# Optimization experiments

Hardware: AMD Instinct MI355X
Metric: run time of the kernel (lower is better)

## Reference

```python
import jax, jax.numpy as jnp
from jax import lax
import numpy as np

COMMITMENT_COST = 0.25
N_EMBED = 512
EDIM = 32


def _conv(x, w, b, stride, pad):
    # x: NCHW, w: OIHW (torch Conv2d layout)
    y = lax.conv_general_dilated(x, w, (stride, stride), [(pad, pad), (pad, pad)],
                                 dimension_numbers=("NCHW", "OIHW", "NCHW"))
    return y + b[None, :, None, None]


def _conv_t(x, w, b, stride, pad):
    # torch ConvTranspose2d weight layout: (in, out, kH, kW)
    k = w.shape[2]
    w_ = jnp.flip(w, (2, 3)).transpose(1, 0, 2, 3)  # -> OIHW
    p = k - 1 - pad
    y = lax.conv_general_dilated(x, w_, (1, 1), [(p, p), (p, p)],
                                 lhs_dilation=(stride, stride),
                                 dimension_numbers=("NCHW", "OIHW", "NCHW"))
    return y + b[None, :, None, None]


def setup_inputs() -> dict:
    key = jax.random.key(0)
    ks = jax.random.split(key, 9)
    rn = lambda k, s: jax.random.normal(k, s, jnp.float32) * 0.05
    return {
        "x": jax.random.normal(ks[0], (32, 3, 256, 256), jnp.float32),
        "e_w1": rn(ks[1], (64, 3, 4, 4)),    "e_b1": jnp.zeros((64,), jnp.float32),
        "e_w2": rn(ks[2], (128, 64, 4, 4)),  "e_b2": jnp.zeros((128,), jnp.float32),
        "e_w3": rn(ks[3], (32, 128, 3, 3)),  "e_b3": jnp.zeros((32,), jnp.float32),
        "embed": jax.random.uniform(ks[4], (N_EMBED, EDIM), jnp.float32,
                                    -1.0 / N_EMBED, 1.0 / N_EMBED),
        "d_w1": rn(ks[5], (32, 128, 3, 3)),  "d_b1": jnp.zeros((128,), jnp.float32),
        "d_w2": rn(ks[6], (128, 64, 4, 4)),  "d_b2": jnp.zeros((64,), jnp.float32),
        "d_w3": rn(ks[7], (64, 3, 4, 4)),    "d_b3": jnp.zeros((3,), jnp.float32),
    }


def reference(x, e_w1, e_b1, e_w2, e_b2, e_w3, e_b3, embed,
              d_w1, d_b1, d_w2, d_b2, d_w3, d_b3):
    # ---- encoder ----
    h = jax.nn.relu(_conv(x, e_w1, e_b1, 2, 1))   # [B,64,128,128]
    h = jax.nn.relu(_conv(h, e_w2, e_b2, 2, 1))   # [B,128,64,64]
    z = jax.nn.relu(_conv(h, e_w3, e_b3, 1, 1))   # [B,32,64,64]
    # ---- vector quantizer ----
    zp = z.transpose(0, 2, 3, 1)                  # BHWC
    zf = zp.reshape(-1, EDIM)                     # [N, 32]
    d = (zf ** 2).sum(1, keepdims=True) + (embed ** 2).sum(1) \
        - 2.0 * zf @ embed.T                      # [N, n_embed]
    idx = jnp.argmin(d, axis=1)                   # [N]
    z_q = embed[idx].reshape(zp.shape)            # gather == onehot @ embed
    sg = lax.stop_gradient
    loss = jnp.mean((sg(z_q) - zp) ** 2) + COMMITMENT_COST * jnp.mean((z_q - sg(zp)) ** 2)
    z_q_st = zp + sg(z_q - zp)                    # straight-through
    z_q_st = z_q_st.transpose(0, 3, 1, 2)         # back to NCHW
    # ---- decoder ----
    h = jax.nn.relu(_conv_t(z_q_st, d_w1, d_b1, 1, 1))  # [B,128,64,64]
    h = jax.nn.relu(_conv_t(h, d_w2, d_b2, 2, 1))       # [B,64,128,128]
    x_recon = _conv_t(h, d_w3, d_b3, 2, 1)              # [B,3,256,256]
    return x_recon, loss
```

## Files before the change

kernel.cpp:

```cpp
#include <hip/hip_runtime.h>


typedef __attribute__((ext_vector_type(8))) short     short8;
typedef __attribute__((ext_vector_type(4))) short     s16x4;
typedef __attribute__((ext_vector_type(8))) __bf16    bf16x8;
typedef __attribute__((ext_vector_type(4))) float     f32x4;
typedef __attribute__((ext_vector_type(4))) unsigned  uint32x4;

#define BATCH 32

__device__ __forceinline__ float b2f(unsigned short b) {
  union { unsigned u; float f; } v; v.u = ((unsigned)b) << 16; return v.f;
}
__device__ __forceinline__ unsigned short f2b(float f) {
  union { float f; unsigned u; } v; v.f = f;
  unsigned r = v.u + 0x7FFF + ((v.u >> 16) & 1);
  return (unsigned short)(r >> 16);
}

__global__ __launch_bounds__(256) void prep1v_k(const float* __restrict__ w,
                                                unsigned short* __restrict__ wq) {
  const int i = blockIdx.x*256 + threadIdx.x;
  const int j = i & 7, l = (i >> 3) & 63, ni = (i >> 9) & 3, ks = i >> 11;
  const int k = ks*32 + (l >> 4)*8 + j;
  const int co = ni*16 + (l & 15);
  wq[i] = (k < 48) ? f2b(w[co*48 + k]) : (unsigned short)0;
}
__global__ __launch_bounds__(256) void prep2v_k(const float* __restrict__ w,
                                                unsigned short* __restrict__ wq) {
  const int i = blockIdx.x*256 + threadIdx.x;
  const int j = i & 7, l = (i >> 3) & 63, ni = (i >> 9) & 7, ks = i >> 12;
  const int lm = l & 15, lk = l >> 4;
  const int tap = ks >> 1, cc = ks & 1;
  const int co = ni*16 + lm, ci = cc*32 + lk*8 + j;
  wq[i] = f2b(w[(co*64 + ci)*16 + tap]);
}
__global__ __launch_bounds__(256) void prep3_k(const float* __restrict__ w,
                                               unsigned short* __restrict__ wq) {
  const int i = blockIdx.x*256 + threadIdx.x;
  const int ci = i & 127, co = (i >> 7) & 31, t = i >> 12;
  wq[i] = f2b(w[(co*128 + ci)*9 + t]);
}
__global__ __launch_bounds__(256) void prep4_k(const float* __restrict__ w,
                                               unsigned short* __restrict__ wq) {
  const int i = blockIdx.x*256 + threadIdx.x;
  const int ci = i & 31, co = (i >> 5) & 127, t = i >> 12;
  wq[i] = f2b(w[(ci*128 + co)*9 + (8 - t)]);
}
__global__ __launch_bounds__(256) void prep5v_k(const float* __restrict__ w,
                                                unsigned short* __restrict__ wq) {
  const int i = blockIdx.x*256 + threadIdx.x;
  const int j = i & 7, l = (i >> 3) & 63, ni = (i >> 9) & 3;
  const int ks = (i >> 11) & 15, p = i >> 15;
  const int lm = l & 15, lk = l >> 4;
  const int py = p >> 1, px = p & 1;
  const int a = ks >> 3, b = (ks >> 2) & 1, cc = ks & 3;
  const int co = ni*16 + lm, ci = cc*32 + lk*8 + j;
  const int ky = 3 - 2*a - py, kx = 3 - 2*b - px;
  wq[i] = f2b(w[(ci*64 + co)*16 + ky*4 + kx]);
}
__global__ __launch_bounds__(256) void prep6_k(const float* __restrict__ w,
                                               unsigned short* __restrict__ wq) {
  const int i = blockIdx.x*256 + threadIdx.x;
  const int j = i & 7, l = (i >> 3) & 63, kc = (i >> 9) & 7, p = i >> 12;
  const int lm = l & 15, lk = l >> 4;
  const int a = kc >> 2, b = (kc >> 1) & 1, ch = kc & 1;
  const int ci = ch*32 + lk*8 + j, co = lm;
  const int py = p >> 1, px = p & 1;
  const int ky = 2 - 2*a + (1 - py), kx = 2 - 2*b + (1 - px);
  wq[i] = (co < 3) ? f2b(w[(ci*3 + co)*16 + ky*4 + kx]) : (unsigned short)0;
}

template<int CIN,int COUT,int HIN,int S,int KW,int NTAPS,int OSTRIDE,int P,
         bool PARITY,bool RELU,bool INF32,bool OUTF32>
__global__ __launch_bounds__(256) void mconv_k(const void* __restrict__ in_,
    const unsigned short* __restrict__ wq_, const float* __restrict__ bias,
    void* __restrict__ out_) {
  constexpr int NF  = COUT / 16;
  constexpr int NCH = CIN / 32;
  __shared__ short Al[128*40];
  __shared__ short Bl[COUT*40];
  int py = 0, px = 0, PY = P, PX = P;
  const unsigned short* wq = wq_;
  if (PARITY) {
    py = blockIdx.y >> 1; px = blockIdx.y & 1;
    PY = 1 - py; PX = 1 - px;
    wq += blockIdx.y * (NTAPS*COUT*CIN);
  }
  const int m0 = blockIdx.x * 128;
  const int w  = threadIdx.x >> 6, l = threadIdx.x & 63;
  const int lm = l & 15, lk = l >> 4;
  f32x4 acc[2][NF];
  #pragma unroll
  for (int mi = 0; mi < 2; ++mi)
    #pragma unroll
    for (int ni = 0; ni < NF; ++ni) acc[mi][ni] = (f32x4)0.0f;

  for (int tap = 0; tap < NTAPS; ++tap) {
    const int ky = tap / KW, kx = tap % KW;
    for (int ch = 0; ch < NCH; ++ch) {
      const int c0 = ch * 32;
      __syncthreads();
      for (int s = threadIdx.x; s < 512; s += 256) {
        const int row = s >> 2, part = s & 3;
        const int m = m0 + row;
        const int n = m >> 12, oy = (m >> 6) & 63, ox = m & 63;
        const int iy = oy*S - PY + ky, ix = ox*S - PX + kx;
        short8 v = (short8)(short)0;
        if (iy >= 0 && iy < HIN && ix >= 0 && ix < HIN) {
          const int base = ((n*HIN + iy)*HIN + ix)*CIN + c0 + part*8;
          if (INF32) {
            const float* pf = (const float*)in_ + base;
            const f32x4 f0 = *(const f32x4*)pf;
            const f32x4 f1 = *(const f32x4*)(pf + 4);
            #pragma unroll
            for (int j = 0; j < 4; ++j) {
              v[j]     = (short)f2b(f0[j]);
              v[j + 4] = (short)f2b(f1[j]);
            }
          } else {
            v = *(const short8*)((const unsigned short*)in_ + base);
          }
        }
        *(short8*)&Al[row*40 + part*8] = v;
      }
      for (int s = threadIdx.x; s < COUT*4; s += 256) {
        const int co = s >> 2, part = s & 3;
        *(short8*)&Bl[co*40 + part*8] =
            *(const short8*)(wq + (tap*COUT + co)*CIN + c0 + part*8);
      }
      __syncthreads();
      short8 av[2];
      #pragma unroll
      for (int mi = 0; mi < 2; ++mi)
        av[mi] = *(const short8*)&Al[(w*32 + mi*16 + lm)*40 + lk*8];
      #pragma unroll
      for (int ni = 0; ni < NF; ++ni) {
        const short8 bv = *(const short8*)&Bl[(ni*16 + lm)*40 + lk*8];
        #pragma unroll
        for (int mi = 0; mi < 2; ++mi)
          acc[mi][ni] = __builtin_amdgcn_mfma_f32_16x16x32_bf16(
              __builtin_bit_cast(bf16x8, av[mi]),
              __builtin_bit_cast(bf16x8, bv),
              acc[mi][ni], 0, 0, 0);
      }
    }
  }
  #pragma unroll
  for (int ni = 0; ni < NF; ++ni) {
    const int co = ni*16 + lm;
    const float bv = bias[co];
    #pragma unroll
    for (int mi = 0; mi < 2; ++mi) {
      #pragma unroll
      for (int r = 0; r < 4; ++r) {
        const int ml = w*32 + mi*16 + lk*4 + r;
        const int m  = m0 + ml;
        float vv = acc[mi][ni][r] + bv;
        if (RELU) vv = fmaxf(vv, 0.f);
        int off;
        if (OSTRIDE == 1) {
          off = m*COUT + co;
        } else {
          const int n = m >> 12, oy = (m >> 6) & 63, ox = m & 63;
          off = ((n*128 + oy*2 + py)*128 + ox*2 + px)*COUT + co;
        }
        if (OUTF32) ((float*)out_)[off] = vv;
        else ((unsigned short*)out_)[off] = f2b(vv);
      }
    }
  }
}

__global__ __launch_bounds__(256) void conv1m_k(const float* __restrict__ x,
    const unsigned short* __restrict__ wv, const float* __restrict__ bias,
    unsigned short* __restrict__ out) {
  __shared__ __align__(16) short RAW[12*264];
  __shared__ __align__(16) short IC[128*64];
  const int wid = ((blockIdx.x & 7) << 9) + (blockIdx.x >> 3);
  const int q = wid & 127, n = wid >> 7;
  for (int i = threadIdx.x; i < 396; i += 256)
    *(short8*)&RAW[i*8] = (short8)(short)0;
  __syncthreads();
  for (int s = threadIdx.x; s < 768; s += 256) {
    const int g = s >> 6, seg = s & 63;
    const int ci = g >> 2, ky = g & 3;
    const int iy = 2*q - 1 + ky;
    if (iy >= 0 && iy < 256) {
      const f32x4 v = *(const f32x4*)&x[((n*3 + ci)*256 + iy)*256 + seg*4];
      s16x4 sv;
      #pragma unroll
      for (int e = 0; e < 4; ++e) sv[e] = (short)f2b(v[e]);
      *(s16x4*)&RAW[g*264 + 4 + seg*4] = sv;
    }
  }
  __syncthreads();
  for (int s = threadIdx.x; s < 1024; s += 256) {
    const int kb = s & 7, ox = s >> 3;
    short8 v = (short8)(short)0;
    if (kb < 6) {
      const unsigned* u0 = (const unsigned*)&RAW[(2*kb  )*264 + 2*ox + 2];
      const unsigned* u1 = (const unsigned*)&RAW[(2*kb+1)*264 + 2*ox + 2];
      const unsigned a0 = u0[0], a1 = u0[1], a2 = u0[2];
      const unsigned b0 = u1[0], b1 = u1[1], b2 = u1[2];
      uint32x4 uv;
      uv[0] = (a0 >> 16) | (a1 << 16);
      uv[1] = (a1 >> 16) | (a2 << 16);
      uv[2] = (b0 >> 16) | (b1 << 16);
      uv[3] = (b1 >> 16) | (b2 << 16);
      v = __builtin_bit_cast(short8, uv);
    }
    const int bo = ((ox << 7) + (kb << 4)) ^ ((ox & 7) << 4);
    *(short8*)((char*)IC + bo) = v;
  }
  __syncthreads();
  const int w = threadIdx.x >> 6, l = threadIdx.x & 63;
  const int lm = l & 15, lk = l >> 4;
  f32x4 acc[2][4];
  #pragma unroll
  for (int mi = 0; mi < 2; ++mi)
    #pragma unroll
    for (int ni = 0; ni < 4; ++ni) acc[mi][ni] = (f32x4)0.0f;
  #pragma unroll
  for (int ks = 0; ks < 2; ++ks) {
    short8 bv[4];
    #pragma unroll
    for (int ni = 0; ni < 4; ++ni)
      bv[ni] = *(const short8*)(wv + (((ks*4 + ni)*64 + l) << 3));
    #pragma unroll
    for (int mi = 0; mi < 2; ++mi) {
      const int ox = w*32 + mi*16 + lm;
      const int bo = ((ox << 7) + (ks << 6) + (lk << 4)) ^ ((ox & 7) << 4);
      const short8 av = *(const short8*)((const char*)IC + bo);
      #pragma unroll
      for (int ni = 0; ni < 4; ++ni)
        acc[mi][ni] = __builtin_amdgcn_mfma_f32_16x16x32_bf16(
            __builtin_bit_cast(bf16x8, av),
            __builtin_bit_cast(bf16x8, bv[ni]),
            acc[mi][ni], 0, 0, 0);
    }
  }
  __syncthreads();
  #pragma unroll
  for (int mi = 0; mi < 2; ++mi)
    #pragma unroll
    for (int ni = 0; ni < 4; ++ni) {
      const int co = ni*16 + lm;
      const float bv = bias[co];
      #pragma unroll
      for (int r = 0; r < 4; ++r) {
        const int ox = w*32 + mi*16 + lk*4 + r;
        const int bo = ((ox << 7) + 2*co) ^ ((ox & 7) << 4);
        *(short*)((char*)IC + bo) = (short)f2b(fmaxf(acc[mi][ni][r] + bv, 0.f));
      }
    }
  __syncthreads();
  const long ob = ((long)(n*128 + q)) * 8192;
  for (int s = threadIdx.x; s < 1024; s += 256) {
    const int kb = s & 7, ox = s >> 3;
    const int bo = ((ox << 7) + (kb << 4)) ^ ((ox & 7) << 4);
    *(short8*)&out[ob + ox*64 + kb*8] = *(const short8*)((const char*)IC + bo);
  }
}

__global__ __launch_bounds__(256) void conv2m_k(const unsigned short* __restrict__ in,
    const unsigned short* __restrict__ wv, const float* __restrict__ bias,
    unsigned short* __restrict__ out) {
  __shared__ short IL[8*66*64];
  const int wid = (blockIdx.x & 7)*256 + (blockIdx.x >> 3);
  const int q = wid & 63, n = wid >> 6;
  for (int i = threadIdx.x; i < 4160; i += 256) {
    const int part = i & 7, t = i >> 3, col = t % 130, r = t / 130;
    const int iy = 2*q - 1 + r, ix = col - 1;
    short8 v = (short8)(short)0;
    if (iy >= 0 && iy < 128 && ix >= 0 && ix < 128)
      v = *(const short8*)(in + (((n*128 + iy)*128 + ix)*64 + part*8));
    const int p = 1 - (ix & 1 ? 0 : 1);
    const int idx = (ix & 1) ? ((ix + 1) >> 1) : (ix >> 1);
    const int bo = ((((r*2 + p)*66 + idx) << 7) + (part << 4)) ^ ((idx & 7) << 4);
    *(short8*)((char*)IL + bo) = v;
  }
  const int w = threadIdx.x >> 6, l = threadIdx.x & 63;
  const int lm = l & 15, lk = l >> 4;
  int Bdc[2][2];
  #pragma unroll
  for (int d = 0; d < 2; ++d) {
    const int xd = ((lm + d) & 7) << 4;
    const int bs = ((lm + d) << 7) + ((lk << 4) ^ (xd & 0x30));
    Bdc[d][0] = bs + (xd & 0x40);
    Bdc[d][1] = bs + ((xd & 0x40) ^ 0x40);
  }
  const unsigned short* wb = wv + w*1024 + l*8;
  __syncthreads();
  f32x4 acc[4][2];
  #pragma unroll
  for (int mi = 0; mi < 4; ++mi)
    #pragma unroll
    for (int ni = 0; ni < 2; ++ni) acc[mi][ni] = (f32x4)0.0f;
  #pragma unroll
  for (int ks = 0; ks < 32; ++ks) {
    const int tap = ks >> 1, cc = ks & 1;
    const int ky = tap >> 2, kx = tap & 3;
    const int p = 1 - (kx & 1), d = kx >> 1;
    short8 bv[2];
    bv[0] = *(const short8*)(wb + ks*4096);
    bv[1] = *(const short8*)(wb + ks*4096 + 512);
    const char* Ab = (const char*)IL + Bdc[d][cc];
    const int imm0 = ((ky*2 + p)*66) << 7;
    #pragma unroll
    for (int mi = 0; mi < 4; ++mi) {
      const short8 av = *(const short8*)(Ab + imm0 + mi*2048);
      #pragma unroll
      for (int ni = 0; ni < 2; ++ni)
        acc[mi][ni] = __builtin_amdgcn_mfma_f32_16x16x32_bf16(
            __builtin_bit_cast(bf16x8, av),
            __builtin_bit_cast(bf16x8, bv[ni]),
            acc[mi][ni], 0, 0, 0);
    }
  }
  #pragma unroll
  for (int mi = 0; mi < 4; ++mi)
    #pragma unroll
    for (int r = 0; r < 4; ++r) {
      const int ox = mi*16 + lk*4 + r;
      const int ob = ((n*64 + q)*64 + ox)*128;
      #pragma unroll
      for (int ni = 0; ni < 2; ++ni) {
        const int co = (w*2 + ni)*16 + lm;
        out[ob + co] = f2b(fmaxf(acc[mi][ni][r] + bias[co], 0.f));
      }
    }
}

__global__ __launch_bounds__(256) void convt2m_k(const unsigned short* __restrict__ in,
    const unsigned short* __restrict__ wv, const float* __restrict__ bias,
    unsigned short* __restrict__ out) {
  __shared__ short IL[3*66*128];
  const int wid = (blockIdx.x & 7)*256 + (blockIdx.x >> 3);
  const int q = wid & 63, n = wid >> 6;
  for (int i = threadIdx.x; i < 3168; i += 256) {
    const int part = i & 15, t = i >> 4, col = t % 66, r = t / 66;
    const int iy = q - 1 + r, ix = col - 1;
    short8 v = (short8)(short)0;
    if (iy >= 0 && iy < 64 && ix >= 0 && ix < 64)
      v = *(const short8*)(in + (((n*64 + iy)*64 + ix)*128 + part*8));
    const int bo = (((r*66 + col) << 8) + (part << 4)) ^ ((col & 7) << 4);
    *(short8*)((char*)IL + bo) = v;
  }
  const int w = threadIdx.x >> 6, l = threadIdx.x & 63;
  const int py = w >> 1, px = w & 1;
  const int lm = l & 15, lk = l >> 4;
  int Wb[2][2];
  #pragma unroll
  for (int b = 0; b < 2; ++b) {
    const int e = lm + px + b;
    const int xb = (e & 7) << 4;
    const int bs = (e << 8) + ((lk << 4) ^ (xb & 0x30));
    Wb[b][0] = bs + (xb & 0x40);
    Wb[b][1] = bs + ((xb & 0x40) ^ 0x40);
  }
  const int pyb = py * 16896;
  const unsigned short* wb = wv + w*32768 + l*8;
  __syncthreads();
  f32x4 acc[4][4];
  #pragma unroll
  for (int mi = 0; mi < 4; ++mi)
    #pragma unroll
    for (int ni = 0; ni < 4; ++ni) acc[mi][ni] = (f32x4)0.0f;
  #pragma unroll
  for (int ks = 0; ks < 16; ++ks) {
    const int a = ks >> 3, b = (ks >> 2) & 1, cc = ks & 3;
    short8 bv[4];
    #pragma unroll
    for (int ni = 0; ni < 4; ++ni)
      bv[ni] = *(const short8*)(wb + ks*2048 + ni*512);
    const char* Ab = (const char*)IL + (pyb + Wb[b][cc & 1]);
    const int imm0 = a*16896 + ((cc >> 1) << 7);
    #pragma unroll
    for (int mi = 0; mi < 4; ++mi) {
      const short8 av = *(const short8*)(Ab + imm0 + mi*4096);
      #pragma unroll
      for (int ni = 0; ni < 4; ++ni)
        acc[mi][ni] = __builtin_amdgcn_mfma_f32_16x16x32_bf16(
            __builtin_bit_cast(bf16x8, av),
            __builtin_bit_cast(bf16x8, bv[ni]),
            acc[mi][ni], 0, 0, 0);
    }
  }
  const int oy = 2*q + py;
  #pragma unroll
  for (int mi = 0; mi < 4; ++mi)
    #pragma unroll
    for (int r = 0; r < 4; ++r) {
      const int ox = 2*(mi*16 + lk*4 + r) + px;
      const int ob = ((n*128 + oy)*128 + ox)*64;
      #pragma unroll
      for (int ni = 0; ni < 4; ++ni) {
        const int co = ni*16 + lm;
        out[ob + co] = f2b(fmaxf(acc[mi][ni][r] + bias[co], 0.f));
      }
    }
}

__global__ __launch_bounds__(256) void vqm_k(const float* __restrict__ z,
    const float* __restrict__ embed, float* __restrict__ zq,
    float* __restrict__ partial) {
  __shared__ short Be[512*40];
  __shared__ float en[512];
  __shared__ int   bidx[128];
  __shared__ float red[256];
  const int m0 = blockIdx.x * 128;
  for (int i = threadIdx.x; i < 4096; i += 256) {
    const int j = i >> 3, k0 = (i & 7) * 4;
    const f32x4 v = *(const f32x4*)&embed[j*32 + k0];
    s16x4 s;
    #pragma unroll
    for (int e = 0; e < 4; ++e) s[e] = (short)f2b(v[e]);
    *(s16x4*)&Be[j*40 + k0] = s;
  }
  __syncthreads();
  for (int j = threadIdx.x; j < 512; j += 256) {
    float s = 0.f;
    #pragma unroll
    for (int q = 0; q < 4; ++q) {
      const short8 v = *(const short8*)&Be[j*40 + q*8];
      #pragma unroll
      for (int e = 0; e < 8; ++e) {
        const float f = b2f((unsigned short)v[e]);
        s = fmaf(f, f, s);
      }
    }
    en[j] = s;
  }
  __syncthreads();
  const int w = threadIdx.x >> 6, l = threadIdx.x & 63;
  const int lm = l & 15, lk = l >> 4;
  const int rw = w * 32;
  short8 av[2];
  #pragma unroll
  for (int mi = 0; mi < 2; ++mi) {
    const float* zp = z + (long)(m0 + rw + mi*16 + lm)*32 + lk*8;
    const f32x4 f0 = *(const f32x4*)zp;
    const f32x4 f1 = *(const f32x4*)(zp + 4);
    short8 v;
    #pragma unroll
    for (int e = 0; e < 4; ++e) {
      v[e]     = (short)f2b(f0[e]);
      v[e + 4] = (short)f2b(f1[e]);
    }
    av[mi] = v;
  }
  float bd[2][4]; int bj[2][4];
  #pragma unroll
  for (int mi = 0; mi < 2; ++mi)
    #pragma unroll
    for (int r = 0; r < 4; ++r) { bd[mi][r] = 1e30f; bj[mi][r] = 0; }
  for (int nc = 0; nc < 8; ++nc) {
    f32x4 acc[2][4];
    #pragma unroll
    for (int mi = 0; mi < 2; ++mi)
      #pragma unroll
      for (int ni = 0; ni < 4; ++ni) acc[mi][ni] = (f32x4)0.0f;
    #pragma unroll
    for (int ni = 0; ni < 4; ++ni) {
      const short8 bv = *(const short8*)&Be[(nc*64 + ni*16 + lm)*40 + lk*8];
      #pragma unroll
      for (int mi = 0; mi < 2; ++mi)
        acc[mi][ni] = __builtin_amdgcn_mfma_f32_16x16x32_bf16(
            __builtin_bit_cast(bf16x8, av[mi]),
            __builtin_bit_cast(bf16x8, bv),
            acc[mi][ni], 0, 0, 0);
    }
    #pragma unroll
    for (int ni = 0; ni < 4; ++ni) {
      const int j = nc*64 + ni*16 + lm;
      const float e_n = en[j];
      #pragma unroll
      for (int mi = 0; mi < 2; ++mi)
        #pragma unroll
        for (int r = 0; r < 4; ++r) {
          const float d = fmaf(-2.f, acc[mi][ni][r], e_n);
          if (d < bd[mi][r]) { bd[mi][r] = d; bj[mi][r] = j; }
        }
    }
  }
  #pragma unroll
  for (int mi = 0; mi < 2; ++mi)
    #pragma unroll
    for (int r = 0; r < 4; ++r) {
      float d = bd[mi][r]; int j = bj[mi][r];
      #pragma unroll
      for (int off = 1; off < 16; off <<= 1) {
        const float od = __shfl_xor(d, off);
        const int   oj = __shfl_xor(j, off);
        if (od < d || (od == d && oj < j)) { d = od; j = oj; }
      }
      if (lm == 0) bidx[rw + mi*16 + lk*4 + r] = j;
    }
  __syncthreads();
  const int pl = threadIdx.x >> 1, hf = (threadIdx.x & 1) * 16;
  const int code = bidx[pl];
  const long pb = (long)(m0 + pl)*32 + hf;
  float se = 0.f;
  #pragma unroll
  for (int q = 0; q < 4; ++q) {
    const f32x4 ev = *(const f32x4*)&embed[code*32 + hf + q*4];
    const f32x4 zv = *(const f32x4*)&z[pb + q*4];
    *(f32x4*)&zq[pb + q*4] = ev;
    const f32x4 df = ev - zv;
    #pragma unroll
    for (int e = 0; e < 4; ++e) se = fmaf(df[e], df[e], se);
  }
  red[threadIdx.x] = se; __syncthreads();
  for (int s = 128; s > 0; s >>= 1) {
    if (threadIdx.x < s) red[threadIdx.x] += red[threadIdx.x + s];
    __syncthreads();
  }
  if (threadIdx.x == 0) partial[blockIdx.x] = red[0];
}

__global__ __launch_bounds__(256) void loss_k(const float* __restrict__ part,
                                              float* __restrict__ out) {
  __shared__ float red[256];
  const int t = threadIdx.x;
  float s = 0.f;
  #pragma unroll
  for (int q = 0; q < 4; ++q) s += part[t + q*256];
  red[t] = s; __syncthreads();
  for (int st = 128; st > 0; st >>= 1) {
    if (t < st) red[t] += red[t + st];
    __syncthreads();
  }
  if (t == 0) out[0] = red[0] * (1.25f / (131072.f * 32.f));
}

__global__ __launch_bounds__(256) void convt3m_k(const unsigned short* __restrict__ in,
    const unsigned short* __restrict__ wq6, const float* __restrict__ bias,
    float* __restrict__ out) {
  __shared__ short8 IL[3*8*66];
  const int h = blockIdx.x & 1, q = (blockIdx.x >> 1) & 127, n = blockIdx.x >> 8;
  for (int i = threadIdx.x; i < 1584; i += 256) {
    const int c8 = i & 7, t = i >> 3, ixl = t % 66, r = t / 66;
    const int iy = q - 1 + r, ix = h*64 - 1 + ixl;
    short8 v = (short8)(short)0;
    if (iy >= 0 && iy < 128 && ix >= 0 && ix < 128)
      v = *(const short8*)(in + (((long)(n*128 + iy)*128 + ix)*64 + c8*8));
    IL[(r*8 + c8)*66 + ixl] = v;
  }
  const int w = threadIdx.x >> 6, l = threadIdx.x & 63;
  const int py = w >> 1, px = w & 1;
  const int lm = l & 15, lk = l >> 4;
  short8 bfrag[8];
  #pragma unroll
  for (int kc = 0; kc < 8; ++kc)
    bfrag[kc] = *(const short8*)(wq6 + (((w*8 + kc)*64 + l) << 3));
  __syncthreads();
  f32x4 acc[4];
  #pragma unroll
  for (int mi = 0; mi < 4; ++mi) acc[mi] = (f32x4)0.0f;
  #pragma unroll
  for (int kc = 0; kc < 8; ++kc) {
    const int a = kc >> 2, b = (kc >> 1) & 1, ch = kc & 1;
    const int base = (((py + a)*8 + ch*4 + lk)*66) + px + b;
    #pragma unroll
    for (int mi = 0; mi < 4; ++mi) {
      const short8 av = *(const short8*)&IL[base + mi*16 + lm];
      acc[mi] = __builtin_amdgcn_mfma_f32_16x16x32_bf16(
          __builtin_bit_cast(bf16x8, av),
          __builtin_bit_cast(bf16x8, bfrag[kc]),
          acc[mi], 0, 0, 0);
    }
  }
  if (lm < 3) {
    const float bv = bias[lm];
    const int oy = 2*q + py;
    const long ob = ((long)(n*3 + lm))*65536 + oy*256;
    #pragma unroll
    for (int mi = 0; mi < 4; ++mi)
      #pragma unroll
      for (int r = 0; r < 4; ++r) {
        const int xq = mi*16 + lk*4 + r;
        out[ob + h*128 + 2*xq + px] = acc[mi][r] + bv;
      }
  }
}

extern "C" void kernel_launch(void* const* d_in, const int* in_sizes, int n_in,
                              void* d_out, int out_size, void* d_ws, size_t ws_size,
                              hipStream_t stream) {
  const float* x   = (const float*)d_in[0];
  const float* ew1 = (const float*)d_in[1];  const float* eb1 = (const float*)d_in[2];
  const float* ew2 = (const float*)d_in[3];  const float* eb2 = (const float*)d_in[4];
  const float* ew3 = (const float*)d_in[5];  const float* eb3 = (const float*)d_in[6];
  const float* emb = (const float*)d_in[7];
  const float* dw1 = (const float*)d_in[8];  const float* db1 = (const float*)d_in[9];
  const float* dw2 = (const float*)d_in[10]; const float* db2 = (const float*)d_in[11];
  const float* dw3 = (const float*)d_in[12]; const float* db3 = (const float*)d_in[13];
  float* out = (float*)d_out;

  uint8_t* w8 = (uint8_t*)d_ws;
  unsigned short* h1 = (unsigned short*)w8;
  unsigned short* h2 = (unsigned short*)(w8 + 67108864);
  float* z   = (float*)(w8 + 100663296);
  float* zq  = (float*)(w8 + 117440512);
  float* part = (float*)(w8 + 67108864);
  unsigned short* wq2 = (unsigned short*)(w8 + 117440512);
  unsigned short* wq3 = (unsigned short*)(w8 + 117440512 + 262144);
  unsigned short* wq1 = (unsigned short*)(w8 + 117440512 + 335872);
  unsigned short* wq4 = (unsigned short*)(w8 + 100663296);
  unsigned short* wq5 = (unsigned short*)(w8 + 100663296 + 73728);
  unsigned short* wq6 = (unsigned short*)(w8 + 100663296 + 335872);
  unsigned short* d1 = h2;
  unsigned short* d2 = h1;

  prep1v_k<<<dim3(16),256,0,stream>>>(ew1, wq1);
  prep2v_k<<<dim3(512),256,0,stream>>>(ew2, wq2);
  prep3_k<<<dim3(144),256,0,stream>>>(ew3, wq3);
  conv1m_k<<<dim3(4096),256,0,stream>>>(x, wq1, eb1, h1);
  conv2m_k<<<dim3(2048),256,0,stream>>>(h1, wq2, eb2, h2);
  mconv_k<128,32,64,1,3,9,1,1,false,true,false,true>
      <<<dim3(1024),256,0,stream>>>(h2, wq3, eb3, z);
  vqm_k<<<dim3(1024),256,0,stream>>>(z, emb, zq, part);
  loss_k<<<dim3(1),256,0,stream>>>(part, out + 6291456);
  prep4_k<<<dim3(144),256,0,stream>>>(dw1, wq4);
  prep5v_k<<<dim3(512),256,0,stream>>>(dw2, wq5);
  prep6_k<<<dim3(64),256,0,stream>>>(dw3, wq6);
  mconv_k<32,128,64,1,3,9,1,1,false,true,true,false>
      <<<dim3(1024),256,0,stream>>>(zq, wq4, db1, d1);
  convt2m_k<<<dim3(2048),256,0,stream>>>(d1, wq5, db2, d2);
  convt3m_k<<<dim3(8192),256,0,stream>>>(d2, wq6, db3, out);
}
```

Measured before the change: 404.5 us.

## Stage conv2 and convT2 input halos in two channel halves to halve LDS

The encoder conv2 and decoder convT2 kernels now load their input halo tiles into shared memory in two channel chunks, computing each chunk's MFMA contributions before loading the next. This halves the LDS footprint per block (about 66KB to 33KB and 50KB to 25KB), which should let more blocks stay resident per CU and hide latency better. The cost is an extra barrier pair per block, serialised load and compute phases inside a block, and changed swizzle layouts. In conv2 the XOR swizzle is dropped, which may cause LDS bank conflicts.

```diff
diff --git a/kernel.cpp b/kernel.cpp
--- a/kernel.cpp
+++ b/kernel.cpp
@@ -266,56 +266,50 @@
 __global__ __launch_bounds__(256) void conv2m_k(const unsigned short* __restrict__ in,
     const unsigned short* __restrict__ wv, const float* __restrict__ bias,
     unsigned short* __restrict__ out) {
-  __shared__ short IL[8*66*64];
+  __shared__ short IL[8*66*32];
   const int wid = (blockIdx.x & 7)*256 + (blockIdx.x >> 3);
   const int q = wid & 63, n = wid >> 6;
-  for (int i = threadIdx.x; i < 4160; i += 256) {
-    const int part = i & 7, t = i >> 3, col = t % 130, r = t / 130;
-    const int iy = 2*q - 1 + r, ix = col - 1;
-    short8 v = (short8)(short)0;
-    if (iy >= 0 && iy < 128 && ix >= 0 && ix < 128)
-      v = *(const short8*)(in + (((n*128 + iy)*128 + ix)*64 + part*8));
-    const int p = 1 - (ix & 1 ? 0 : 1);
-    const int idx = (ix & 1) ? ((ix + 1) >> 1) : (ix >> 1);
-    const int bo = ((((r*2 + p)*66 + idx) << 7) + (part << 4)) ^ ((idx & 7) << 4);
-    *(short8*)((char*)IL + bo) = v;
-  }
   const int w = threadIdx.x >> 6, l = threadIdx.x & 63;
   const int lm = l & 15, lk = l >> 4;
-  int Bdc[2][2];
-  #pragma unroll
-  for (int d = 0; d < 2; ++d) {
-    const int xd = ((lm + d) & 7) << 4;
-    const int bs = ((lm + d) << 7) + ((lk << 4) ^ (xd & 0x30));
-    Bdc[d][0] = bs + (xd & 0x40);
-    Bdc[d][1] = bs + ((xd & 0x40) ^ 0x40);
-  }
+  const int Bd0 = lm*64 + lk*16;
   const unsigned short* wb = wv + w*1024 + l*8;
-  __syncthreads();
   f32x4 acc[4][2];
   #pragma unroll
   for (int mi = 0; mi < 4; ++mi)
     #pragma unroll
     for (int ni = 0; ni < 2; ++ni) acc[mi][ni] = (f32x4)0.0f;
   #pragma unroll
-  for (int ks = 0; ks < 32; ++ks) {
-    const int tap = ks >> 1, cc = ks & 1;
-    const int ky = tap >> 2, kx = tap & 3;
-    const int p = 1 - (kx & 1), d = kx >> 1;
-    short8 bv[2];
-    bv[0] = *(const short8*)(wb + ks*4096);
-    bv[1] = *(const short8*)(wb + ks*4096 + 512);
-    const char* Ab = (const char*)IL + Bdc[d][cc];
-    const int imm0 = ((ky*2 + p)*66) << 7;
-    #pragma unroll
-    for (int mi = 0; mi < 4; ++mi) {
-      const short8 av = *(const short8*)(Ab + imm0 + mi*2048);
-      #pragma unroll
-      for (int ni = 0; ni < 2; ++ni)
-        acc[mi][ni] = __builtin_amdgcn_mfma_f32_16x16x32_bf16(
-            __builtin_bit_cast(bf16x8, av),
-            __builtin_bit_cast(bf16x8, bv[ni]),
-            acc[mi][ni], 0, 0, 0);
+  for (int c = 0; c < 2; ++c) {
+    if (c) __syncthreads();
+    for (int i = threadIdx.x; i < 2112; i += 256) {
+      const int part = i & 3, e = i >> 2;
+      const int idx = e % 66, rp = e / 66;
+      const int r = rp >> 1, p = rp & 1;
+      const int iy = 2*q - 1 + r, ix = 2*idx - p;
+      short8 v = (short8)(short)0;
+      if (iy >= 0 && iy < 128 && ix >= 0 && ix < 128)
+        v = *(const short8*)(in + (((n*128 + iy)*128 + ix)*64 + c*32 + part*8));
+      *(short8*)&IL[e*32 + part*8] = v;
+    }
+    __syncthreads();
+    #pragma unroll
+    for (int t = 0; t < 16; ++t) {
+      const int ky = t >> 2, kx = t & 3;
+      const int p = 1 - (kx & 1), d = kx >> 1;
+      const short8 bv0 = *(const short8*)(wb + (t*2 + c)*4096);
+      const short8 bv1 = *(const short8*)(wb + (t*2 + c)*4096 + 512);
+      const char* Ab = (const char*)IL + (Bd0 + d*64);
+      const int imm0 = ((ky*2 + p)*66) << 6;
+      #pragma unroll
+      for (int mi = 0; mi < 4; ++mi) {
+        const short8 av = *(const short8*)(Ab + imm0 + mi*1024);
+        acc[mi][0] = __builtin_amdgcn_mfma_f32_16x16x32_bf16(
+            __builtin_bit_cast(bf16x8, av), __builtin_bit_cast(bf16x8, bv0),
+            acc[mi][0], 0, 0, 0);
+        acc[mi][1] = __builtin_amdgcn_mfma_f32_16x16x32_bf16(
+            __builtin_bit_cast(bf16x8, av), __builtin_bit_cast(bf16x8, bv1),
+            acc[mi][1], 0, 0, 0);
+      }
     }
   }
   #pragma unroll
@@ -335,18 +329,9 @@
 __global__ __launch_bounds__(256) void convt2m_k(const unsigned short* __restrict__ in,
     const unsigned short* __restrict__ wv, const float* __restrict__ bias,
     unsigned short* __restrict__ out) {
-  __shared__ short IL[3*66*128];
+  __shared__ short IL[3*66*64];
   const int wid = (blockIdx.x & 7)*256 + (blockIdx.x >> 3);
   const int q = wid & 63, n = wid >> 6;
-  for (int i = threadIdx.x; i < 3168; i += 256) {
-    const int part = i & 15, t = i >> 4, col = t % 66, r = t / 66;
-    const int iy = q - 1 + r, ix = col - 1;
-    short8 v = (short8)(short)0;
-    if (iy >= 0 && iy < 64 && ix >= 0 && ix < 64)
-      v = *(const short8*)(in + (((n*64 + iy)*64 + ix)*128 + part*8));
-    const int bo = (((r*66 + col) << 8) + (part << 4)) ^ ((col & 7) << 4);
-    *(short8*)((char*)IL + bo) = v;
-  }
   const int w = threadIdx.x >> 6, l = threadIdx.x & 63;
   const int py = w >> 1, px = w & 1;
   const int lm = l & 15, lk = l >> 4;
@@ -354,37 +339,50 @@
   #pragma unroll
   for (int b = 0; b < 2; ++b) {
     const int e = lm + px + b;
-    const int xb = (e & 7) << 4;
-    const int bs = (e << 8) + ((lk << 4) ^ (xb & 0x30));
-    Wb[b][0] = bs + (xb & 0x40);
-    Wb[b][1] = bs + ((xb & 0x40) ^ 0x40);
-  }
-  const int pyb = py * 16896;
+    Wb[b][0] = (e << 7) + ((lk << 4) ^ ((e & 7) << 4));
+    Wb[b][1] = Wb[b][0] ^ 0x40;
+  }
+  const int pyb = py * 8448;
   const unsigned short* wb = wv + w*32768 + l*8;
-  __syncthreads();
   f32x4 acc[4][4];
   #pragma unroll
   for (int mi = 0; mi < 4; ++mi)
     #pragma unroll
     for (int ni = 0; ni < 4; ++ni) acc[mi][ni] = (f32x4)0.0f;
   #pragma unroll
-  for (int ks = 0; ks < 16; ++ks) {
-    const int a = ks >> 3, b = (ks >> 2) & 1, cc = ks & 3;
-    short8 bv[4];
-    #pragma unroll
-    for (int ni = 0; ni < 4; ++ni)
-      bv[ni] = *(const short8*)(wb + ks*2048 + ni*512);
-    const char* Ab = (const char*)IL + (pyb + Wb[b][cc & 1]);
-    const int imm0 = a*16896 + ((cc >> 1) << 7);
-    #pragma unroll
-    for (int mi = 0; mi < 4; ++mi) {
-      const short8 av = *(const short8*)(Ab + imm0 + mi*4096);
+  for (int c = 0; c < 2; ++c) {
+    if (c) __syncthreads();
+    for (int i = threadIdx.x; i < 1584; i += 256) {
+      const int part = i & 7, e = i >> 3;
+      const int col = e % 66, r = e / 66;
+      const int iy = q - 1 + r, ix = col - 1;
+      short8 v = (short8)(short)0;
+      if (iy >= 0 && iy < 64 && ix >= 0 && ix < 64)
+        v = *(const short8*)(in + (((n*64 + iy)*64 + ix)*128 + c*64 + part*8));
+      const int bo = (e << 7) + ((part << 4) ^ ((col & 7) << 4));
+      *(short8*)((char*)IL + bo) = v;
+    }
+    __syncthreads();
+    #pragma unroll
+    for (int u = 0; u < 8; ++u) {
+      const int a = u >> 2, b = (u >> 1) & 1, c1 = u & 1;
+      const int ks = (a << 3) | (b << 2) | (2*c + c1);
+      short8 bv[4];
       #pragma unroll
       for (int ni = 0; ni < 4; ++ni)
-        acc[mi][ni] = __builtin_amdgcn_mfma_f32_16x16x32_bf16(
-            __builtin_bit_cast(bf16x8, av),
-            __builtin_bit_cast(bf16x8, bv[ni]),
-            acc[mi][ni], 0, 0, 0);
+        bv[ni] = *(const short8*)(wb + ks*2048 + ni*512);
+      const char* Ab = (const char*)IL + (pyb + Wb[b][c1]);
+      const int imm0 = a*8448;
+      #pragma unroll
+      for (int mi = 0; mi < 4; ++mi) {
+        const short8 av = *(const short8*)(Ab + imm0 + mi*2048);
+        #pragma unroll
+        for (int ni = 0; ni < 4; ++ni)
+          acc[mi][ni] = __builtin_amdgcn_mfma_f32_16x16x32_bf16(
+              __builtin_bit_cast(bf16x8, av),
+              __builtin_bit_cast(bf16x8, bv[ni]),
+              acc[mi][ni], 0, 0, 0);
+      }
     }
   }
   const int oy = 2*q + py;
```

After: 391.1 us. -3.3%, faster.
